# Kernel tuning notes

Measured on AMD Instinct MI355X. Metric: run time of the kernel, lower is better.

Reference implementation:

```python
import jax, jax.numpy as jnp
import numpy as np
from jax import lax

B, TPI, C = 16, 20, 80      # batch, targets per image, num classes
IMG = 1280.0
STRIDES = (8, 16, 32)
EPS_LS = 0.05               # label smoothing eps


def setup_inputs():
    key = jax.random.key(0)
    k1, k2, k3, k4, k5, k6 = jax.random.split(key, 6)
    grids, strides = [], []
    for s in STRIDES:
        n = int(IMG // s)
        gy, gx = jnp.meshgrid(jnp.arange(n, dtype=jnp.float32), jnp.arange(n, dtype=jnp.float32), indexing='ij')
        grids.append(jnp.stack([gx.ravel(), gy.ravel()], -1))
        strides.append(jnp.full((n * n,), float(s), jnp.float32))
    grid_mask = jnp.concatenate(grids, 0)        # (A,2)
    stride_mask = jnp.concatenate(strides, 0)    # (A,)
    A = grid_mask.shape[0]
    # predictions: valid xyxy boxes + (obj, cls) logits
    ctr = jax.random.uniform(k1, (B, A, 2), minval=0., maxval=IMG)
    wh = jax.random.uniform(k2, (B, A, 2), minval=10., maxval=200.)
    boxes = jnp.concatenate([ctr - wh / 2, ctr + wh / 2], -1)
    logits = jax.random.normal(k3, (B, A, 1 + C)) * 2.0
    preds = jnp.concatenate([boxes, logits], -1)  # (B,A,4+1+C)
    # targets: exactly TPI rows per image, sorted by image id: <img_id, cid, x1,y1,x2,y2>
    img_id = jnp.repeat(jnp.arange(B, dtype=jnp.float32), TPI)
    cid = jax.random.randint(k4, (B * TPI,), 0, C).astype(jnp.float32)
    tctr = jax.random.uniform(k5, (B * TPI, 2), minval=100., maxval=IMG - 100.)
    twh = jax.random.uniform(k6, (B * TPI, 2), minval=40., maxval=300.)
    tbox = jnp.concatenate([tctr - twh / 2, tctr + twh / 2], -1)
    targets = jnp.concatenate([img_id[:, None], cid[:, None], tbox], -1)
    return {"preds": preds, "grid_mask": grid_mask, "stride_mask": stride_mask, "targets": targets}


def _box_iou(a, b):
    # a: (T,4), b: (A,4) xyxy -> (T,A)
    area_a = (a[:, 2] - a[:, 0]) * (a[:, 3] - a[:, 1])
    area_b = (b[:, 2] - b[:, 0]) * (b[:, 3] - b[:, 1])
    lt = jnp.maximum(a[:, None, :2], b[None, :, :2])
    rb = jnp.minimum(a[:, None, 2:], b[None, :, 2:])
    wh = jnp.clip(rb - lt, 0.)
    inter = wh[..., 0] * wh[..., 1]
    return inter / (area_a[:, None] + area_b[None, :] - inter + 1e-8)


def _ciou(a, b):
    # elementwise complete-IoU, a/b: (N,4) xyxy -> (N,)
    lt = jnp.maximum(a[:, :2], b[:, :2])
    rb = jnp.minimum(a[:, 2:], b[:, 2:])
    wh = jnp.clip(rb - lt, 0.)
    inter = wh[:, 0] * wh[:, 1]
    wa, ha = a[:, 2] - a[:, 0], a[:, 3] - a[:, 1]
    wb, hb = b[:, 2] - b[:, 0], b[:, 3] - b[:, 1]
    union = wa * ha + wb * hb - inter + 1e-7
    iou = inter / union
    cw = jnp.maximum(a[:, 2], b[:, 2]) - jnp.minimum(a[:, 0], b[:, 0])
    ch = jnp.maximum(a[:, 3], b[:, 3]) - jnp.minimum(a[:, 1], b[:, 1])
    c2 = cw * cw + ch * ch + 1e-7
    rho2 = ((a[:, 0] + a[:, 2] - b[:, 0] - b[:, 2]) ** 2 + (a[:, 1] + a[:, 3] - b[:, 1] - b[:, 3]) ** 2) / 4.
    v = (4. / (jnp.pi ** 2)) * (jnp.arctan(wb / (hb + 1e-7)) - jnp.arctan(wa / (ha + 1e-7))) ** 2
    alpha = lax.stop_gradient(v / (1. - iou + v + 1e-7))
    return iou - rho2 / c2 - alpha * v


def _assign_image(p, tgt, valid, grid, stride):
    # p: (A,5+C), tgt: (T,6), valid: (T,) bool
    K = 10
    T = tgt.shape[0]
    A = p.shape[0]
    xc = (grid[:, 0] + 0.5) * stride  # (A,)
    yc = (grid[:, 1] + 0.5) * stride
    x1, y1, x2, y2 = tgt[:, 2:3], tgt[:, 3:4], tgt[:, 4:5], tgt[:, 5:6]  # (T,1)
    deltas = jnp.stack([xc[None] - x1, yc[None] - y1, x2 - xc[None], y2 - yc[None]], -1)  # (T,A,4)
    in_boxes = (jnp.min(deltas, -1) > 0.) & valid[:, None]
    cxt, cyt = (x1 + x2) / 2, (y1 + y2) / 2
    in_centers = (jnp.maximum(jnp.abs(xc[None] - cxt), jnp.abs(yc[None] - cyt)) < 2.5 * stride[None]) & valid[:, None]
    fg = (in_boxes | in_centers).any(0)           # (A,) is_in_boxes_or_center
    is_matched = in_boxes & in_centers            # (T,A)
    iou = _box_iou(tgt[:, 2:], p[:, :4])          # (T,A)
    prob = jnp.sqrt(jax.nn.sigmoid(p[:, 4:5]) * jax.nn.sigmoid(p[:, 5:]))
    prob = jnp.clip(prob, 1e-7, 1. - 1e-7)        # (A,C)
    y = jax.nn.one_hot(tgt[:, 1].astype(jnp.int32), C) * valid[:, None].astype(jnp.float32)  # (T,C)
    # BCE summed over classes without materializing (T,A,C): matmul over C
    cls_cost = -(y @ jnp.log(prob).T + (1. - y) @ jnp.log1p(-prob).T)  # (T,A)
    cost = (cls_cost - 3. * jnp.log(iou + 1e-8)
            + 1e5 * (~is_matched) + 1e6 * (~fg)[None] + 1e9 * (~valid)[:, None])
    # dynamic-k: sum of top-10 IoUs over fg anchors, truncated to int, >=1
    topk_iou, _ = lax.top_k(jnp.where(fg[None], iou, 0.), K)
    dyn_k = jnp.clip(topk_iou.sum(1).astype(jnp.int32), 1, K)
    _, idx = lax.top_k(-cost, K)  # smallest-cost anchors per target
    sel = (jnp.arange(K)[None] < dyn_k[:, None]) & valid[:, None]
    mm = jnp.zeros((T, A), bool).at[jnp.arange(T)[:, None], idx].set(sel)
    mm = mm & fg[None]
    # resolve anchors claimed by multiple targets: keep min-cost target
    multi = mm.sum(0) > 1
    argmin_t = jnp.argmin(cost, 0)  # (A,)
    mm = jnp.where(multi[None], jnp.arange(T)[:, None] == argmin_t[None], mm)
    matched = mm.any(0)             # (A,) final obj target (aliased fg in original)
    at = jnp.argmax(mm, 0)          # (A,) assigned target per anchor
    pred_ious = (mm * iou).sum(0)   # (A,)
    reg = tgt[at, 2:] * matched[:, None].astype(jnp.float32)
    cls_t = jax.nn.one_hot(tgt[at, 1].astype(jnp.int32), C) * pred_ious[:, None] * matched[:, None].astype(jnp.float32)
    return reg, matched, cls_t


def _assign_batch(preds, grid, stride, targets):
    Bn = preds.shape[0]
    tgt = targets.reshape(Bn, -1, 6)
    valid = tgt[..., 0].astype(jnp.int32) == jnp.arange(Bn)[:, None]
    reg, obj, cls_t = jax.vmap(lambda p, t, v: _assign_image(p, t, v, grid, stride))(preds, tgt, valid)
    return reg.reshape(-1, 4), obj.reshape(-1), cls_t.reshape(-1, C)


def _bce_logits(z, y):
    return jnp.maximum(z, 0.) - z * y + jnp.log1p(jnp.exp(-jnp.abs(z)))


def reference(preds, grid_mask, stride_mask, targets):
    reg, obj, cls_t = lax.stop_gradient(_assign_batch(preds, grid_mask, stride_mask, targets))
    pf = preds.reshape(-1, preds.shape[-1])  # (B*A, 5+C)
    objf = obj.astype(pf.dtype)
    npos = jnp.maximum(objf.sum(), 1.)
    # lbox: mean over matched anchors of (1 - CIoU)
    safe_reg = jnp.where(obj[:, None], reg, pf[:, :4])
    lbox = ((1. - _ciou(pf[:, :4], safe_reg)) * objf).sum() / npos
    # lobj: BCE-with-logits on class logits vs smoothed iou-scaled one-hot, matched anchors
    cls_s = jnp.where(cls_t > 0., 1. - EPS_LS, EPS_LS / (C - 1))
    lobj = (_bce_logits(pf[:, 5:], cls_s) * objf[:, None]).sum() / (npos * C)
    # lcls: BCE-with-logits on objectness logit vs matched mask, all anchors
    lcls = _bce_logits(pf[:, 4], objf).mean()
    total = lbox + lobj + lcls
    return total, jnp.stack([lbox, lobj, lcls])
```

## Files before the change

### kernel.cpp

```cpp
#include <hip/hip_runtime.h>
#include <cstdint>
#include <cstddef>

#define BDIM 256
constexpr int Bn = 16;
constexpr int Tn = 20;
constexpr int Cn = 80;
constexpr int An = 33600;
constexpr int BA = Bn * An;
constexpr int NBLK_C = BA / BDIM;
constexpr int SL = 8;
constexpr int ANB = An / SL;
constexpr int CAP = 2048;
constexpr int MCAP = 4096;
constexpr int BLK_PER_IMG = An * 8 / BDIM;

__device__ __forceinline__ float sigm(float x) { return 1.0f / (1.0f + expf(-x)); }
__device__ __forceinline__ float bce(float z, float y) {
    return fmaxf(z, 0.0f) - z * y + log1pf(expf(-fabsf(z)));
}

constexpr float LOG2E = 1.4426950408889634f;
constexpr float LN2   = 0.6931471805599453f;
__device__ __forceinline__ float fexp2(float x){ float r; asm("v_exp_f32 %0, %1" : "=v"(r) : "v"(x)); return r; }
__device__ __forceinline__ float flog2(float x){ float r; asm("v_log_f32 %0, %1" : "=v"(r) : "v"(x)); return r; }
__device__ __forceinline__ float frcp (float x){ float r; asm("v_rcp_f32 %0, %1" : "=v"(r) : "v"(x)); return r; }
__device__ __forceinline__ float fsqrt(float x){ float r; asm("v_sqrt_f32 %0, %1" : "=v"(r) : "v"(x)); return r; }
__device__ __forceinline__ float fsigm(float z){ return frcp(1.0f + fexp2(-z * LOG2E)); }
__device__ __forceinline__ float flogn(float x){ return flog2(x) * LN2; }

__device__ __forceinline__ uint32_t fkey(float f) {
    uint32_t b = __float_as_uint(f);
    return (b & 0x80000000u) ? ~b : (b | 0x80000000u);
}
__device__ __forceinline__ uint32_t unfkey(uint32_t u) {
    return (u & 0x80000000u) ? (u & 0x7FFFFFFFu) : ~u;
}
__device__ __forceinline__ uint64_t wmin64(uint64_t x) {
#pragma unroll
    for (int off = 1; off < 64; off <<= 1) {
        uint64_t o = (uint64_t)__shfl_xor((unsigned long long)x, off);
        x = (o < x) ? o : x;
    }
    return x;
}
__device__ __forceinline__ uint64_t wmax64(uint64_t x) {
#pragma unroll
    for (int off = 1; off < 64; off <<= 1) {
        uint64_t o = (uint64_t)__shfl_xor((unsigned long long)x, off);
        x = (o > x) ? o : x;
    }
    return x;
}

__global__ __launch_bounds__(BDIM) void phaseA(
    const float* __restrict__ preds, const float* __restrict__ grid,
    const float* __restrict__ strd, const float* __restrict__ tgt,
    float4* __restrict__ box4, float* __restrict__ sobjv, float* __restrict__ objzv,
    float* __restrict__ Sbuf, uint32_t* __restrict__ fgim,
    uint32_t* __restrict__ mm, int* __restrict__ cnt, int* __restrict__ mcnt)
{
    __shared__ float tT[Tn * 6];
    int tid = threadIdx.x;
    int b = blockIdx.x / BLK_PER_IMG;
    if (tid < Tn * 6) tT[tid] = tgt[b * Tn * 6 + tid];
    if (blockIdx.x == 0) {
        for (int i = tid; i < Bn * Tn; i += BDIM) cnt[i] = 0;
        if (tid == 0) *mcnt = 0;
    }
    __syncthreads();

    int idx = blockIdx.x * BDIM + tid;
    int g = idx >> 3, q = idx & 7;
    int a = g - b * An;
    const float* r = preds + (size_t)g * 85;

    float objz = r[4];
    float sobj = fsigm(objz);
    float S2 = 0.0f;
#pragma unroll
    for (int cc = 0; cc < 10; ++cc) {
        int c = q + 8 * cc;
        float z = r[5 + c];
        float pr = fsqrt(sobj * fsigm(z));
        pr = fminf(fmaxf(pr, 1e-7f), 1.0f - 1e-7f);
        S2 += flog2(1.0f - pr);
    }
    S2 += __shfl_xor(S2, 1);
    S2 += __shfl_xor(S2, 2);
    S2 += __shfl_xor(S2, 4);

    float gx = grid[a * 2], gy = grid[a * 2 + 1], sv = strd[a];
    float xc = (gx + 0.5f) * sv, yc = (gy + 0.5f) * sv;
    uint32_t im_p = 0, fg_p = 0;
#pragma unroll
    for (int k = 0; k < 3; ++k) {
        int t = q + 8 * k;
        if (t < Tn) {
            const float* trr = tT + t * 6;
            bool valid = ((int)trr[0] == b);
            float x1 = trr[2], y1 = trr[3], x2 = trr[4], y2 = trr[5];
            float dmin = fminf(fminf(xc - x1, yc - y1), fminf(x2 - xc, y2 - yc));
            bool inb = (dmin > 0.0f) && valid;
            float cxt = (x1 + x2) * 0.5f, cyt = (y1 + y2) * 0.5f;
            bool inc = (fmaxf(fabsf(xc - cxt), fabsf(yc - cyt)) < 2.5f * sv) && valid;
            if (inb || inc) fg_p = 1u;
            if (inb && inc) im_p |= (1u << t);
        }
    }
    im_p |= __shfl_xor(im_p, 1); im_p |= __shfl_xor(im_p, 2); im_p |= __shfl_xor(im_p, 4);
    fg_p |= __shfl_xor(fg_p, 1); fg_p |= __shfl_xor(fg_p, 2); fg_p |= __shfl_xor(fg_p, 4);

    if (q == 0) {
        box4[g] = make_float4(r[0], r[1], r[2], r[3]);
        sobjv[g] = sobj; objzv[g] = objz; Sbuf[g] = S2 * LN2;
        fgim[g] = im_p | (fg_p ? 0x80000000u : 0u);
        mm[g] = 0u;
    }
}

__global__ __launch_bounds__(BDIM) void phaseBs(
    const float* __restrict__ tgt, const float4* __restrict__ box4,
    const uint32_t* __restrict__ fgim,
    int* __restrict__ cnt, int* __restrict__ candIdx, float* __restrict__ candV)
{
    int bt = blockIdx.x / SL, sl = blockIdx.x % SL;
    int b = bt / Tn, t = bt % Tn;
    const float* tr = tgt + (size_t)bt * 6;
    if ((int)tr[0] != b) return;
    float tx1 = tr[2], ty1 = tr[3], tx2 = tr[4], ty2 = tr[5];
    float areaT = (tx2 - tx1) * (ty2 - ty1);
    int tid = threadIdx.x;
    int baseg = b * An;
    uint32_t tmask = 1u << t;

    float V[10];
#pragma unroll
    for (int j = 0; j < 10; ++j) V[j] = 0.0f;

    int aend = (sl + 1) * ANB;
    for (int a = sl * ANB + tid; a < aend; a += BDIM) {
        int g = baseg + a;
        uint32_t fi = fgim[g];
        if (fi & tmask) {
            int pos = atomicAdd(&cnt[bt], 1);
            if (pos < CAP) candIdx[bt * CAP + pos] = a;
        }
        if (fi & 0x80000000u) {
            float4 pb = box4[g];
            float areaP = (pb.z - pb.x) * (pb.w - pb.y);
            float w = fmaxf(fminf(tx2, pb.z) - fmaxf(tx1, pb.x), 0.0f);
            float h = fmaxf(fminf(ty2, pb.w) - fmaxf(ty1, pb.y), 0.0f);
            float inter = w * h;
            float iou = inter / (areaT + areaP - inter + 1e-8f);
            if (iou > V[9]) {
                V[9] = iou;
#pragma unroll
                for (int j = 9; j > 0; --j) {
                    float hi = fmaxf(V[j-1], V[j]), lo = fminf(V[j-1], V[j]);
                    V[j-1] = hi; V[j] = lo;
                }
            }
        }
    }

    int lane = tid & 63, wid = tid >> 6;
    __shared__ float wTop[4][10];
    float out[10];
#pragma unroll
    for (int r = 0; r < 10; ++r) {
        uint64_t pk = ((uint64_t)fkey(V[0]) << 32) | (uint32_t)lane;
        pk = wmax64(pk);
        int wl = (int)(pk & 63u);
        out[r] = __shfl(V[0], wl);
        bool win = (lane == wl);
#pragma unroll
        for (int j = 0; j < 9; ++j) V[j] = win ? V[j+1] : V[j];
        V[9] = win ? -1.0f : V[9];
    }
    if (lane == 0) {
#pragma unroll
        for (int r = 0; r < 10; ++r) wTop[wid][r] = out[r];
    }
    __syncthreads();
    if (wid == 0) {
        float x = (lane < 40) ? wTop[lane / 10][lane % 10] : -1.0f;
        int base_out = bt * (SL * 10) + sl * 10;
#pragma unroll
        for (int r = 0; r < 10; ++r) {
            uint64_t pk = ((uint64_t)fkey(x) << 32) | (uint32_t)lane;
            pk = wmax64(pk);
            int wl = (int)(pk & 63u);
            float v = __shfl(x, wl);
            if (lane == 0) candV[base_out + r] = v;
            if (lane == wl) x = -1.0f;
        }
    }
}

__global__ __launch_bounds__(BDIM) void phaseBc(
    const float* __restrict__ preds, const float* __restrict__ tgt,
    const float4* __restrict__ box4, const float* __restrict__ sobjv,
    const float* __restrict__ Sbuf, const uint32_t* __restrict__ fgim,
    const int* __restrict__ cnt, const int* __restrict__ candIdx,
    const float* __restrict__ candV, uint32_t* __restrict__ mm,
    int* __restrict__ mcnt, int* __restrict__ mlist)
{
    int bt = blockIdx.x;
    int b = bt / Tn, t = bt % Tn;
    const float* tr = tgt + (size_t)bt * 6;
    if ((int)tr[0] != b) return;
    int ct = (int)tr[1];
    float tx1 = tr[2], ty1 = tr[3], tx2 = tr[4], ty2 = tr[5];
    float areaT = (tx2 - tx1) * (ty2 - ty1);
    int tid = threadIdx.x, lane = tid & 63, wid = tid >> 6;
    int baseg = b * An;
    int M = cnt[bt];
    bool slow = (M < 10) || (M > CAP);

    uint64_t L[10];
#pragma unroll
    for (int j = 0; j < 10; ++j) L[j] = ~0ULL;

    if (!slow) {
        for (int i = tid; i < M; i += BDIM) {
            int a = candIdx[bt * CAP + i];
            int g = baseg + a;
            float4 pb = box4[g];
            float areaP = (pb.z - pb.x) * (pb.w - pb.y);
            float w = fmaxf(fminf(tx2, pb.z) - fmaxf(tx1, pb.x), 0.0f);
            float h = fmaxf(fminf(ty2, pb.w) - fmaxf(ty1, pb.y), 0.0f);
            float inter = w * h;
            float iou = inter / (areaT + areaP - inter + 1e-8f);
            float z = preds[(size_t)g * 85 + 5 + ct];
            float pr = fsqrt(sobjv[g] * fsigm(z));
            pr = fminf(fmaxf(pr, 1e-7f), 1.0f - 1e-7f);
            float clsc = -(flogn(pr) + Sbuf[g] - flogn(1.0f - pr));
            float cost = clsc - 3.0f * flogn(iou + 1e-8f);
            uint64_t k = ((uint64_t)fkey(cost) << 32) | (uint32_t)a;
            uint64_t m9 = (k < L[9]) ? k : L[9];
            L[9] = m9;
#pragma unroll
            for (int j = 9; j > 0; --j) {
                uint64_t lo = (L[j-1] < L[j]) ? L[j-1] : L[j];
                uint64_t hi = (L[j-1] < L[j]) ? L[j] : L[j-1];
                L[j-1] = lo; L[j] = hi;
            }
        }
    } else {
        for (int a = tid; a < An; a += BDIM) {
            int g = baseg + a;
            uint32_t fi = fgim[g];
            float4 pb = box4[g];
            float areaP = (pb.z - pb.x) * (pb.w - pb.y);
            float w = fmaxf(fminf(tx2, pb.z) - fmaxf(tx1, pb.x), 0.0f);
            float h = fmaxf(fminf(ty2, pb.w) - fmaxf(ty1, pb.y), 0.0f);
            float inter = w * h;
            float iou = inter / (areaT + areaP - inter + 1e-8f);
            float z = preds[(size_t)g * 85 + 5 + ct];
            float pr = fsqrt(sobjv[g] * fsigm(z));
            pr = fminf(fmaxf(pr, 1e-7f), 1.0f - 1e-7f);
            float clsc = -(flogn(pr) + Sbuf[g] - flogn(1.0f - pr));
            float cost = clsc - 3.0f * flogn(iou + 1e-8f)
                       + (((fi >> t) & 1u) ? 0.0f : 100000.0f)
                       + ((fi & 0x80000000u) ? 0.0f : 1000000.0f);
            uint64_t k = ((uint64_t)fkey(cost) << 32) | (uint32_t)a;
            uint64_t m9 = (k < L[9]) ? k : L[9];
            L[9] = m9;
#pragma unroll
            for (int j = 9; j > 0; --j) {
                uint64_t lo = (L[j-1] < L[j]) ? L[j-1] : L[j];
                uint64_t hi = (L[j-1] < L[j]) ? L[j] : L[j-1];
                L[j-1] = lo; L[j] = hi;
            }
        }
    }

    __shared__ uint64_t wT[4][10];
    __shared__ int s_sel[10];
    __shared__ int s_dynk;
    uint64_t wout[10];
#pragma unroll
    for (int r = 0; r < 10; ++r) {
        uint64_t m = wmin64(L[0]);
        wout[r] = m;
        bool win = (L[0] == m) && (m != ~0ULL);
#pragma unroll
        for (int j = 0; j < 9; ++j) L[j] = win ? L[j+1] : L[j];
        L[9] = win ? ~0ULL : L[9];
    }
    if (lane == 0) {
#pragma unroll
        for (int r = 0; r < 10; ++r) wT[wid][r] = wout[r];
    }
    __syncthreads();
    if (wid == 0) {
        uint64_t x = (lane < 40) ? wT[lane / 10][lane % 10] : ~0ULL;
#pragma unroll
        for (int r = 0; r < 10; ++r) {
            uint64_t m = wmin64(x);
            if (lane == 0) s_sel[r] = (int)(m & 0xFFFFFFFFu);
            if (x == m && m != ~0ULL) x = ~0ULL;
        }
        const float* cv = candV + bt * (SL * 10);
        float v0 = cv[lane];
        float v1 = (lane < SL * 10 - 64) ? cv[lane + 64] : -1.0f;
        float accum = 0.0f;
#pragma unroll
        for (int r = 0; r < 10; ++r) {
            bool p0 = (v0 >= v1);
            float hv = p0 ? v0 : v1;
            uint32_t slot = p0 ? (uint32_t)lane : (uint32_t)(lane + 64);
            uint64_t pk = ((uint64_t)fkey(hv) << 32) | slot;
            pk = wmax64(pk);
            int ws = (int)(pk & 127u);
            float v = __uint_as_float(unfkey((uint32_t)(pk >> 32)));
            accum += v;
            if (ws == lane) v0 = -1.0f;
            else if (ws == lane + 64) v1 = -1.0f;
        }
        if (lane == 0) {
            int dynk = (int)accum;
            s_dynk = min(max(dynk, 1), 10);
        }
    }
    __syncthreads();
    if (tid < s_dynk) {
        int a = s_sel[tid];
        int g = baseg + a;
        if (fgim[g] & 0x80000000u) {
            if (atomicOr((unsigned int*)&mm[g], 1u << t) == 0u) {
                int pos = atomicAdd(mcnt, 1);
                if (pos < MCAP) mlist[pos] = g;
            }
        }
    }
}

__global__ __launch_bounds__(BDIM) void phaseD(
    const float* __restrict__ preds, const float* __restrict__ tgt,
    const float4* __restrict__ box4, const float* __restrict__ sobjv,
    const float* __restrict__ Sbuf, const uint32_t* __restrict__ fgim,
    const uint32_t* __restrict__ mm, const int* __restrict__ mcnt,
    const int* __restrict__ mlist,
    float* __restrict__ lboxA, float* __restrict__ lobjA)
{
    __shared__ float tT[Bn * Tn * 6];
    for (int i = threadIdx.x; i < Bn * Tn * 6; i += BDIM) tT[i] = tgt[i];
    __syncthreads();

    int n = min(*mcnt, MCAP);
    for (int i = blockIdx.x * BDIM + threadIdx.x; i < n; i += gridDim.x * BDIM) {
        int g = mlist[i];
        int b = g / An;
        float4 pb = box4[g];
        float px1 = pb.x, py1 = pb.y, px2 = pb.z, py2 = pb.w;
        uint32_t m = mm[g];
        int pc = __popc(m);

        int at; float pred_iou;
        if (pc == 1) {
            at = __ffs(m) - 1;
            const float* trr = tT + (b * Tn + at) * 6;
            float tx1 = trr[2], ty1 = trr[3], tx2 = trr[4], ty2 = trr[5];
            float areaT = (tx2 - tx1) * (ty2 - ty1);
            float areaP = (px2 - px1) * (py2 - py1);
            float w = fmaxf(fminf(tx2, px2) - fmaxf(tx1, px1), 0.0f);
            float h = fmaxf(fminf(ty2, py2) - fmaxf(ty1, py1), 0.0f);
            float inter = w * h;
            pred_iou = inter / (areaT + areaP - inter + 1e-8f);
        } else {
            float S = Sbuf[g];
            uint32_t fi = fgim[g];
            float sobj = sobjv[g];
            float areaP = (px2 - px1) * (py2 - py1);
            float best = INFINITY;
            at = -1; pred_iou = 0.0f;
            for (int t = 0; t < Tn; ++t) {
                const float* trr = tT + (b * Tn + t) * 6;
                bool valid = ((int)trr[0] == b);
                int ctt = (int)trr[1];
                float tx1 = trr[2], ty1 = trr[3], tx2 = trr[4], ty2 = trr[5];
                float areaT = (tx2 - tx1) * (ty2 - ty1);
                float w = fmaxf(fminf(tx2, px2) - fmaxf(tx1, px1), 0.0f);
                float h = fmaxf(fminf(ty2, py2) - fmaxf(ty1, py1), 0.0f);
                float inter = w * h;
                float iou = inter / (areaT + areaP - inter + 1e-8f);
                float z = preds[(size_t)g * 85 + 5 + ctt];
                float pr = fsqrt(sobj * fsigm(z));
                pr = fminf(fmaxf(pr, 1e-7f), 1.0f - 1e-7f);
                float clsc = valid ? -(flogn(pr) + S - flogn(1.0f - pr)) : -S;
                float cost = clsc - 3.0f * flogn(iou + 1e-8f)
                           + (((fi >> t) & 1u) ? 0.0f : 100000.0f)
                           + ((fi & 0x80000000u) ? 0.0f : 1000000.0f)
                           + (valid ? 0.0f : 1000000000.0f);
                if (cost < best) { best = cost; at = t; pred_iou = iou; }
            }
        }

        const float* trr = tT + (b * Tn + at) * 6;
        float bx1 = trr[2], by1 = trr[3], bx2 = trr[4], by2 = trr[5];
        float w = fmaxf(fminf(px2, bx2) - fmaxf(px1, bx1), 0.0f);
        float h = fmaxf(fminf(py2, by2) - fmaxf(py1, by1), 0.0f);
        float inter = w * h;
        float wa = px2 - px1, ha = py2 - py1, wb = bx2 - bx1, hb = by2 - by1;
        float uni = wa * ha + wb * hb - inter + 1e-7f;
        float iou = inter / uni;
        float cw = fmaxf(px2, bx2) - fminf(px1, bx1);
        float ch = fmaxf(py2, by2) - fminf(py1, by1);
        float c2 = cw * cw + ch * ch + 1e-7f;
        float dx = px1 + px2 - bx1 - bx2, dy = py1 + py2 - by1 - by2;
        float rho2 = (dx * dx + dy * dy) / 4.0f;
        float dat = atanf(wb / (hb + 1e-7f)) - atanf(wa / (ha + 1e-7f));
        float v = 0.4052847345693511f * dat * dat;
        float alpha = v / (1.0f - iou + v + 1e-7f);
        float ciou = iou - rho2 / c2 - alpha * v;

        int cls = (int)trr[1];
        bool pos = (pred_iou > 0.0f);
        const float* zp = preds + (size_t)g * 85 + 5;
        float lo = 0.0f;
        for (int c0 = 0; c0 < Cn; c0 += 8) {
            float z[8];
#pragma unroll
            for (int j = 0; j < 8; ++j) z[j] = zp[c0 + j];
#pragma unroll
            for (int j = 0; j < 8; ++j) {
                float y = (pos && (c0 + j) == cls) ? 0.95f : 6.329113924050633e-4f;
                lo += bce(z[j], y);
            }
        }
        lboxA[g] = 1.0f - ciou;
        lobjA[g] = lo;
    }
}

__global__ __launch_bounds__(BDIM) void phaseE(
    const float* __restrict__ objzv, const uint32_t* __restrict__ mm,
    const float* __restrict__ lboxA, const float* __restrict__ lobjA,
    float* __restrict__ pLbox, float* __restrict__ pLobj,
    float* __restrict__ pLcls, float* __restrict__ pNpos)
{
    int tid = threadIdx.x;
    int g = blockIdx.x * BDIM + tid;
    uint32_t m = mm[g];
    bool matched = (m != 0u);
    float lbox_i = matched ? lboxA[g] : 0.0f;
    float lobj_i = matched ? lobjA[g] : 0.0f;
    float npos_i = matched ? 1.0f : 0.0f;
    float lcls_i = bce(objzv[g], matched ? 1.0f : 0.0f);

    __shared__ float red4[4][BDIM];
    red4[0][tid] = lbox_i; red4[1][tid] = lobj_i;
    red4[2][tid] = lcls_i; red4[3][tid] = npos_i;
    __syncthreads();
    for (int s = BDIM / 2; s > 0; s >>= 1) {
        if (tid < s) {
            red4[0][tid] += red4[0][tid + s];
            red4[1][tid] += red4[1][tid + s];
            red4[2][tid] += red4[2][tid + s];
            red4[3][tid] += red4[3][tid + s];
        }
        __syncthreads();
    }
    if (tid == 0) {
        pLbox[blockIdx.x] = red4[0][0];
        pLobj[blockIdx.x] = red4[1][0];
        pLcls[blockIdx.x] = red4[2][0];
        pNpos[blockIdx.x] = red4[3][0];
    }
}

__global__ __launch_bounds__(BDIM) void finalK(
    const float* __restrict__ pLbox, const float* __restrict__ pLobj,
    const float* __restrict__ pLcls, const float* __restrict__ pNpos,
    float* __restrict__ out)
{
    int tid = threadIdx.x;
    float s0 = 0, s1 = 0, s2 = 0, s3 = 0;
    for (int i = tid; i < NBLK_C; i += BDIM) {
        s0 += pLbox[i]; s1 += pLobj[i]; s2 += pLcls[i]; s3 += pNpos[i];
    }
    __shared__ float red4[4][BDIM];
    red4[0][tid] = s0; red4[1][tid] = s1; red4[2][tid] = s2; red4[3][tid] = s3;
    __syncthreads();
    for (int s = BDIM / 2; s > 0; s >>= 1) {
        if (tid < s) {
            red4[0][tid] += red4[0][tid + s];
            red4[1][tid] += red4[1][tid + s];
            red4[2][tid] += red4[2][tid + s];
            red4[3][tid] += red4[3][tid + s];
        }
        __syncthreads();
    }
    if (tid == 0) {
        float npos = fmaxf(red4[3][0], 1.0f);
        float lbox = red4[0][0] / npos;
        float lobj = red4[1][0] / (npos * (float)Cn);
        float lcls = red4[2][0] / (float)(Bn * An);
        out[0] = lbox + lobj + lcls;
        out[1] = lbox;
        out[2] = lobj;
        out[3] = lcls;
    }
}

extern "C" void kernel_launch(void* const* d_in, const int* in_sizes, int n_in,
                              void* d_out, int out_size, void* d_ws, size_t ws_size,
                              hipStream_t stream)
{
    (void)in_sizes; (void)n_in; (void)out_size; (void)ws_size;
    const float* preds = (const float*)d_in[0];
    const float* grid  = (const float*)d_in[1];
    const float* strd  = (const float*)d_in[2];
    const float* tgt   = (const float*)d_in[3];

    char* ws = (char*)d_ws;
    float4*   box4  = (float4*)ws;   ws += (size_t)BA * 16;
    float*    sobjv = (float*)ws;    ws += (size_t)BA * 4;
    float*    objzv = (float*)ws;    ws += (size_t)BA * 4;
    float*    Sbuf  = (float*)ws;    ws += (size_t)BA * 4;
    uint32_t* fgim  = (uint32_t*)ws; ws += (size_t)BA * 4;
    uint32_t* mm    = (uint32_t*)ws; ws += (size_t)BA * 4;
    int*      cnt   = (int*)ws;      ws += (size_t)Bn * Tn * 4;
    int*      mcnt  = (int*)ws;      ws += 16;
    int*   mlist   = (int*)ws;       ws += (size_t)MCAP * 4;
    float* lboxA   = (float*)ws;     ws += (size_t)BA * 4;
    float* lobjA   = (float*)ws;     ws += (size_t)BA * 4;
    int*   candIdx = (int*)ws;       ws += (size_t)Bn * Tn * CAP * 4;
    float* candV   = (float*)ws;     ws += (size_t)Bn * Tn * SL * 10 * 4;
    float* pLbox = (float*)ws;       ws += (size_t)NBLK_C * 4;
    float* pLobj = (float*)ws;       ws += (size_t)NBLK_C * 4;
    float* pLcls = (float*)ws;       ws += (size_t)NBLK_C * 4;
    float* pNpos = (float*)ws;       ws += (size_t)NBLK_C * 4;

    phaseA<<<Bn * BLK_PER_IMG, BDIM, 0, stream>>>(preds, grid, strd, tgt,
                                                  box4, sobjv, objzv, Sbuf, fgim,
                                                  mm, cnt, mcnt);
    phaseBs<<<Bn * Tn * SL, BDIM, 0, stream>>>(tgt, box4, fgim, cnt, candIdx, candV);
    phaseBc<<<Bn * Tn, BDIM, 0, stream>>>(preds, tgt, box4, sobjv, Sbuf, fgim,
                                          cnt, candIdx, candV, mm, mcnt, mlist);
    phaseD<<<32, BDIM, 0, stream>>>(preds, tgt, box4, sobjv, Sbuf, fgim, mm,
                                    mcnt, mlist, lboxA, lobjA);
    phaseE<<<NBLK_C, BDIM, 0, stream>>>(objzv, mm, lboxA, lobjA,
                                        pLbox, pLobj, pLcls, pNpos);
    finalK<<<1, BDIM, 0, stream>>>(pLbox, pLobj, pLcls, pNpos, (float*)d_out);
}
```

Before: 130.8 us.

## Fuse candidate scan into per-target assignment kernel and fold final reduction

```diff
diff --git a/kernel.cpp b/kernel.cpp
--- a/kernel.cpp
+++ b/kernel.cpp
@@ -9,13 +9,10 @@
 constexpr int An = 33600;
 constexpr int BA = Bn * An;
 constexpr int NBLK_C = BA / BDIM;
-constexpr int SL = 8;
-constexpr int ANB = An / SL;
-constexpr int CAP = 2048;
 constexpr int MCAP = 4096;
+constexpr int LCAP = 128;
 constexpr int BLK_PER_IMG = An * 8 / BDIM;
 
-__device__ __forceinline__ float sigm(float x) { return 1.0f / (1.0f + expf(-x)); }
 __device__ __forceinline__ float bce(float z, float y) {
     return fmaxf(z, 0.0f) - z * y + log1pf(expf(-fabsf(z)));
 }
@@ -58,16 +55,13 @@
     const float* __restrict__ strd, const float* __restrict__ tgt,
     float4* __restrict__ box4, float* __restrict__ sobjv, float* __restrict__ objzv,
     float* __restrict__ Sbuf, uint32_t* __restrict__ fgim,
-    uint32_t* __restrict__ mm, int* __restrict__ cnt, int* __restrict__ mcnt)
+    uint32_t* __restrict__ mm, int* __restrict__ mcnt, int* __restrict__ done)
 {
     __shared__ float tT[Tn * 6];
     int tid = threadIdx.x;
     int b = blockIdx.x / BLK_PER_IMG;
     if (tid < Tn * 6) tT[tid] = tgt[b * Tn * 6 + tid];
-    if (blockIdx.x == 0) {
-        for (int i = tid; i < Bn * Tn; i += BDIM) cnt[i] = 0;
-        if (tid == 0) *mcnt = 0;
-    }
+    if (blockIdx.x == 0 && tid == 0) { *mcnt = 0; *done = 0; }
     __syncthreads();
 
     int idx = blockIdx.x * BDIM + tid;
@@ -119,92 +113,11 @@
     }
 }
 
-__global__ __launch_bounds__(BDIM) void phaseBs(
-    const float* __restrict__ tgt, const float4* __restrict__ box4,
-    const uint32_t* __restrict__ fgim,
-    int* __restrict__ cnt, int* __restrict__ candIdx, float* __restrict__ candV)
-{
-    int bt = blockIdx.x / SL, sl = blockIdx.x % SL;
-    int b = bt / Tn, t = bt % Tn;
-    const float* tr = tgt + (size_t)bt * 6;
-    if ((int)tr[0] != b) return;
-    float tx1 = tr[2], ty1 = tr[3], tx2 = tr[4], ty2 = tr[5];
-    float areaT = (tx2 - tx1) * (ty2 - ty1);
-    int tid = threadIdx.x;
-    int baseg = b * An;
-    uint32_t tmask = 1u << t;
-
-    float V[10];
-#pragma unroll
-    for (int j = 0; j < 10; ++j) V[j] = 0.0f;
-
-    int aend = (sl + 1) * ANB;
-    for (int a = sl * ANB + tid; a < aend; a += BDIM) {
-        int g = baseg + a;
-        uint32_t fi = fgim[g];
-        if (fi & tmask) {
-            int pos = atomicAdd(&cnt[bt], 1);
-            if (pos < CAP) candIdx[bt * CAP + pos] = a;
-        }
-        if (fi & 0x80000000u) {
-            float4 pb = box4[g];
-            float areaP = (pb.z - pb.x) * (pb.w - pb.y);
-            float w = fmaxf(fminf(tx2, pb.z) - fmaxf(tx1, pb.x), 0.0f);
-            float h = fmaxf(fminf(ty2, pb.w) - fmaxf(ty1, pb.y), 0.0f);
-            float inter = w * h;
-            float iou = inter / (areaT + areaP - inter + 1e-8f);
-            if (iou > V[9]) {
-                V[9] = iou;
-#pragma unroll
-                for (int j = 9; j > 0; --j) {
-                    float hi = fmaxf(V[j-1], V[j]), lo = fminf(V[j-1], V[j]);
-                    V[j-1] = hi; V[j] = lo;
-                }
-            }
-        }
-    }
-
-    int lane = tid & 63, wid = tid >> 6;
-    __shared__ float wTop[4][10];
-    float out[10];
-#pragma unroll
-    for (int r = 0; r < 10; ++r) {
-        uint64_t pk = ((uint64_t)fkey(V[0]) << 32) | (uint32_t)lane;
-        pk = wmax64(pk);
-        int wl = (int)(pk & 63u);
-        out[r] = __shfl(V[0], wl);
-        bool win = (lane == wl);
-#pragma unroll
-        for (int j = 0; j < 9; ++j) V[j] = win ? V[j+1] : V[j];
-        V[9] = win ? -1.0f : V[9];
-    }
-    if (lane == 0) {
-#pragma unroll
-        for (int r = 0; r < 10; ++r) wTop[wid][r] = out[r];
-    }
-    __syncthreads();
-    if (wid == 0) {
-        float x = (lane < 40) ? wTop[lane / 10][lane % 10] : -1.0f;
-        int base_out = bt * (SL * 10) + sl * 10;
-#pragma unroll
-        for (int r = 0; r < 10; ++r) {
-            uint64_t pk = ((uint64_t)fkey(x) << 32) | (uint32_t)lane;
-            pk = wmax64(pk);
-            int wl = (int)(pk & 63u);
-            float v = __shfl(x, wl);
-            if (lane == 0) candV[base_out + r] = v;
-            if (lane == wl) x = -1.0f;
-        }
-    }
-}
-
-__global__ __launch_bounds__(BDIM) void phaseBc(
+__global__ __launch_bounds__(BDIM) void phaseB(
     const float* __restrict__ preds, const float* __restrict__ tgt,
     const float4* __restrict__ box4, const float* __restrict__ sobjv,
     const float* __restrict__ Sbuf, const uint32_t* __restrict__ fgim,
-    const int* __restrict__ cnt, const int* __restrict__ candIdx,
-    const float* __restrict__ candV, uint32_t* __restrict__ mm,
-    int* __restrict__ mcnt, int* __restrict__ mlist)
+    uint32_t* __restrict__ mm, int* __restrict__ mcnt, int* __restrict__ mlist)
 {
     int bt = blockIdx.x;
     int b = bt / Tn, t = bt % Tn;
@@ -215,16 +128,70 @@
     float areaT = (tx2 - tx1) * (ty2 - ty1);
     int tid = threadIdx.x, lane = tid & 63, wid = tid >> 6;
     int baseg = b * An;
-    int M = cnt[bt];
-    bool slow = (M < 10) || (M > CAP);
+    uint32_t tmask = 1u << t;
+
+    __shared__ int s_cnt;
+    __shared__ int s_cand[LCAP];
+    if (tid == 0) s_cnt = 0;
+    __syncthreads();
+
+    float V[10];
+#pragma unroll
+    for (int j = 0; j < 10; ++j) V[j] = 0.0f;
+    for (int a = tid; a < An; a += BDIM) {
+        int g = baseg + a;
+        uint32_t fi = fgim[g];
+        if (fi & tmask) {
+            int p = atomicAdd(&s_cnt, 1);
+            if (p < LCAP) s_cand[p] = a;
+        }
+        if (fi & 0x80000000u) {
+            float4 pb = box4[g];
+            float areaP = (pb.z - pb.x) * (pb.w - pb.y);
+            float w = fmaxf(fminf(tx2, pb.z) - fmaxf(tx1, pb.x), 0.0f);
+            float h = fmaxf(fminf(ty2, pb.w) - fmaxf(ty1, pb.y), 0.0f);
+            float inter = w * h;
+            float iou = inter / (areaT + areaP - inter + 1e-8f);
+            if (iou > V[9]) {
+                V[9] = iou;
+#pragma unroll
+                for (int j = 9; j > 0; --j) {
+                    float hi = fmaxf(V[j-1], V[j]), lo = fminf(V[j-1], V[j]);
+                    V[j-1] = hi; V[j] = lo;
+                }
+            }
+        }
+    }
+    __syncthreads();
+    int M = s_cnt;
+
+    __shared__ float wTop[4][10];
+    {
+        float out[10];
+#pragma unroll
+        for (int r = 0; r < 10; ++r) {
+            uint64_t pk = ((uint64_t)fkey(V[0]) << 32) | (uint32_t)lane;
+            pk = wmax64(pk);
+            int wl = (int)(pk & 63u);
+            out[r] = __shfl(V[0], wl);
+            bool win = (lane == wl);
+#pragma unroll
+            for (int j = 0; j < 9; ++j) V[j] = win ? V[j+1] : V[j];
+            V[9] = win ? -1.0f : V[9];
+        }
+        if (lane == 0) {
+#pragma unroll
+            for (int r = 0; r < 10; ++r) wTop[wid][r] = out[r];
+        }
+    }
 
     uint64_t L[10];
 #pragma unroll
     for (int j = 0; j < 10; ++j) L[j] = ~0ULL;
-
+    bool slow = (M < 10) || (M > LCAP);
     if (!slow) {
         for (int i = tid; i < M; i += BDIM) {
-            int a = candIdx[bt * CAP + i];
+            int a = s_cand[i];
             int g = baseg + a;
             float4 pb = box4[g];
             float areaP = (pb.z - pb.x) * (pb.w - pb.y);
@@ -279,19 +246,21 @@
     __shared__ uint64_t wT[4][10];
     __shared__ int s_sel[10];
     __shared__ int s_dynk;
-    uint64_t wout[10];
-#pragma unroll
-    for (int r = 0; r < 10; ++r) {
-        uint64_t m = wmin64(L[0]);
-        wout[r] = m;
-        bool win = (L[0] == m) && (m != ~0ULL);
-#pragma unroll
-        for (int j = 0; j < 9; ++j) L[j] = win ? L[j+1] : L[j];
-        L[9] = win ? ~0ULL : L[9];
-    }
-    if (lane == 0) {
-#pragma unroll
-        for (int r = 0; r < 10; ++r) wT[wid][r] = wout[r];
+    {
+        uint64_t wout[10];
+#pragma unroll
+        for (int r = 0; r < 10; ++r) {
+            uint64_t m = wmin64(L[0]);
+            wout[r] = m;
+            bool win = (L[0] == m) && (m != ~0ULL);
+#pragma unroll
+            for (int j = 0; j < 9; ++j) L[j] = win ? L[j+1] : L[j];
+            L[9] = win ? ~0ULL : L[9];
+        }
+        if (lane == 0) {
+#pragma unroll
+            for (int r = 0; r < 10; ++r) wT[wid][r] = wout[r];
+        }
     }
     __syncthreads();
     if (wid == 0) {
@@ -302,22 +271,15 @@
             if (lane == 0) s_sel[r] = (int)(m & 0xFFFFFFFFu);
             if (x == m && m != ~0ULL) x = ~0ULL;
         }
-        const float* cv = candV + bt * (SL * 10);
-        float v0 = cv[lane];
-        float v1 = (lane < SL * 10 - 64) ? cv[lane + 64] : -1.0f;
+        float xv = (lane < 40) ? wTop[lane / 10][lane % 10] : -1.0f;
         float accum = 0.0f;
 #pragma unroll
         for (int r = 0; r < 10; ++r) {
-            bool p0 = (v0 >= v1);
-            float hv = p0 ? v0 : v1;
-            uint32_t slot = p0 ? (uint32_t)lane : (uint32_t)(lane + 64);
-            uint64_t pk = ((uint64_t)fkey(hv) << 32) | slot;
+            uint64_t pk = ((uint64_t)fkey(xv) << 32) | (uint32_t)lane;
             pk = wmax64(pk);
-            int ws = (int)(pk & 127u);
-            float v = __uint_as_float(unfkey((uint32_t)(pk >> 32)));
-            accum += v;
-            if (ws == lane) v0 = -1.0f;
-            else if (ws == lane + 64) v1 = -1.0f;
+            int slot = (int)(pk & 0xFFFFFFFFu);
+            accum += __uint_as_float(unfkey((uint32_t)(pk >> 32)));
+            if (lane == slot) xv = -1.0f;
         }
         if (lane == 0) {
             int dynk = (int)accum;
@@ -435,11 +397,12 @@
     }
 }
 
-__global__ __launch_bounds__(BDIM) void phaseE(
+__global__ __launch_bounds__(BDIM) void phaseEF(
     const float* __restrict__ objzv, const uint32_t* __restrict__ mm,
     const float* __restrict__ lboxA, const float* __restrict__ lobjA,
     float* __restrict__ pLbox, float* __restrict__ pLobj,
-    float* __restrict__ pLcls, float* __restrict__ pNpos)
+    float* __restrict__ pLcls, float* __restrict__ pNpos,
+    int* __restrict__ done, float* __restrict__ out)
 {
     int tid = threadIdx.x;
     int g = blockIdx.x * BDIM + tid;
@@ -463,25 +426,24 @@
         }
         __syncthreads();
     }
+    __shared__ int s_last;
     if (tid == 0) {
         pLbox[blockIdx.x] = red4[0][0];
         pLobj[blockIdx.x] = red4[1][0];
         pLcls[blockIdx.x] = red4[2][0];
         pNpos[blockIdx.x] = red4[3][0];
-    }
-}
-
-__global__ __launch_bounds__(BDIM) void finalK(
-    const float* __restrict__ pLbox, const float* __restrict__ pLobj,
-    const float* __restrict__ pLcls, const float* __restrict__ pNpos,
-    float* __restrict__ out)
-{
-    int tid = threadIdx.x;
+        __threadfence();
+        int old = atomicAdd(done, 1);
+        s_last = (old == NBLK_C - 1) ? 1 : 0;
+    }
+    __syncthreads();
+    if (!s_last) return;
+    __threadfence();
+
     float s0 = 0, s1 = 0, s2 = 0, s3 = 0;
     for (int i = tid; i < NBLK_C; i += BDIM) {
         s0 += pLbox[i]; s1 += pLobj[i]; s2 += pLcls[i]; s3 += pNpos[i];
     }
-    __shared__ float red4[4][BDIM];
     red4[0][tid] = s0; red4[1][tid] = s1; red4[2][tid] = s2; red4[3][tid] = s3;
     __syncthreads();
     for (int s = BDIM / 2; s > 0; s >>= 1) {
@@ -522,13 +484,11 @@
     float*    Sbuf  = (float*)ws;    ws += (size_t)BA * 4;
     uint32_t* fgim  = (uint32_t*)ws; ws += (size_t)BA * 4;
     uint32_t* mm    = (uint32_t*)ws; ws += (size_t)BA * 4;
-    int*      cnt   = (int*)ws;      ws += (size_t)Bn * Tn * 4;
     int*      mcnt  = (int*)ws;      ws += 16;
+    int*      done  = (int*)ws;      ws += 16;
     int*   mlist   = (int*)ws;       ws += (size_t)MCAP * 4;
     float* lboxA   = (float*)ws;     ws += (size_t)BA * 4;
     float* lobjA   = (float*)ws;     ws += (size_t)BA * 4;
-    int*   candIdx = (int*)ws;       ws += (size_t)Bn * Tn * CAP * 4;
-    float* candV   = (float*)ws;     ws += (size_t)Bn * Tn * SL * 10 * 4;
     float* pLbox = (float*)ws;       ws += (size_t)NBLK_C * 4;
     float* pLobj = (float*)ws;       ws += (size_t)NBLK_C * 4;
     float* pLcls = (float*)ws;       ws += (size_t)NBLK_C * 4;
@@ -536,13 +496,12 @@
 
     phaseA<<<Bn * BLK_PER_IMG, BDIM, 0, stream>>>(preds, grid, strd, tgt,
                                                   box4, sobjv, objzv, Sbuf, fgim,
-                                                  mm, cnt, mcnt);
-    phaseBs<<<Bn * Tn * SL, BDIM, 0, stream>>>(tgt, box4, fgim, cnt, candIdx, candV);
-    phaseBc<<<Bn * Tn, BDIM, 0, stream>>>(preds, tgt, box4, sobjv, Sbuf, fgim,
-                                          cnt, candIdx, candV, mm, mcnt, mlist);
+                                                  mm, mcnt, done);
+    phaseB<<<Bn * Tn, BDIM, 0, stream>>>(preds, tgt, box4, sobjv, Sbuf, fgim,
+                                         mm, mcnt, mlist);
     phaseD<<<32, BDIM, 0, stream>>>(preds, tgt, box4, sobjv, Sbuf, fgim, mm,
                                     mcnt, mlist, lboxA, lobjA);
-    phaseE<<<NBLK_C, BDIM, 0, stream>>>(objzv, mm, lboxA, lobjA,
-                                        pLbox, pLobj, pLcls, pNpos);
-    finalK<<<1, BDIM, 0, stream>>>(pLbox, pLobj, pLcls, pNpos, (float*)d_out);
-}
+    phaseEF<<<NBLK_C, BDIM, 0, stream>>>(objzv, mm, lboxA, lobjA,
+                                         pLbox, pLobj, pLcls, pNpos,
+                                         done, (float*)d_out);
+}
```

After: 218.6 us. 1.67x slower.
